# Kernel tuning notes

Measured on AMD Instinct MI355X. Metric: run time of the kernel, lower is better.

Reference implementation:

```python
import jax, jax.numpy as jnp
import numpy as np
from jax import lax

VOCAB = 60      # len(ALL_CHARS): BOS + 52 letters + " .,;'-" + EOS
EMB = 100       # emb_dim
HID = 100       # HIDDEN_SIZE
SEQ = 262144    # long-document sequence length


def setup_inputs() -> dict:
    key = jax.random.key(0)
    k = jax.random.split(key, 6)
    s = 1.0 / np.sqrt(HID)  # PyTorch GRU init scale
    x = jax.random.randint(k[0], (1, SEQ), 0, VOCAB)
    emb = jax.random.normal(k[1], (VOCAB, EMB), dtype=jnp.float32)
    w_ih = jax.random.uniform(k[2], (3 * HID, EMB), minval=-s, maxval=s, dtype=jnp.float32)
    w_hh = jax.random.uniform(k[3], (3 * HID, HID), minval=-s, maxval=s, dtype=jnp.float32)
    b_ih = jax.random.uniform(k[4], (3 * HID,), minval=-s, maxval=s, dtype=jnp.float32)
    b_hh = jax.random.uniform(k[5], (3 * HID,), minval=-s, maxval=s, dtype=jnp.float32)
    return {"x": x, "emb": emb, "w_ih": w_ih, "w_hh": w_hh, "b_ih": b_ih, "b_hh": b_hh}


def reference(x, emb, w_ih, w_hh, b_ih, b_hh):
    # Embedding lookup: [1, S] -> [S, E]  (batch asserted == 1 in original)
    xe = emb[x[0]]
    # Precompute input-side gate projections for all timesteps: [S, 3H]
    xp = xe @ w_ih.T + b_ih
    H = w_hh.shape[1]
    w_hr, w_hz, w_hn = w_hh[:H], w_hh[H:2 * H], w_hh[2 * H:]
    b_hr, b_hz, b_hn = b_hh[:H], b_hh[H:2 * H], b_hh[2 * H:]

    def step(h, xp_t):
        xr, xz, xn = xp_t[:H], xp_t[H:2 * H], xp_t[2 * H:]
        r = jax.nn.sigmoid(xr + h @ w_hr.T + b_hr)
        z = jax.nn.sigmoid(xz + h @ w_hz.T + b_hz)
        n = jnp.tanh(xn + r * (h @ w_hn.T + b_hn))
        h_new = (1.0 - z) * n + z * h
        return h_new, None

    h0 = jnp.zeros((H,), dtype=xp.dtype)
    h_last, _ = lax.scan(step, h0, xp)
    # Match torch GRU h_n shape: [num_layers=1, batch=1, HID]
    return h_last[None, None, :]
```

## Files before the change

### kernel.cpp

```cpp
#include <hip/hip_runtime.h>
#include <stdint.h>

#define VOCAB 60
#define EMB   100
#define HID   100
#define SEQN  262144
#define NPROJ 300
#define HSTR  104
#define NMFW  4
#define MT    6
#define KS    3

typedef float    f32x4 __attribute__((ext_vector_type(4)));
typedef _Float16 h16x2 __attribute__((ext_vector_type(2)));
typedef _Float16 h16x4 __attribute__((ext_vector_type(4)));
typedef _Float16 h16x8 __attribute__((ext_vector_type(8)));

__device__ __forceinline__ float fast_sig(float x) {
    return __builtin_amdgcn_rcpf(1.0f + __builtin_amdgcn_exp2f(-1.442695041f * x));
}
__device__ __forceinline__ float fast_tanh(float x) {
    return 2.0f * __builtin_amdgcn_rcpf(1.0f + __builtin_amdgcn_exp2f(-2.885390082f * x)) - 1.0f;
}

#if __has_builtin(__builtin_amdgcn_fdot2)
#define DOT2(A, B, C) __builtin_amdgcn_fdot2((A), (B), (C), false)
#else
__device__ __forceinline__ float DOT2(h16x2 a, h16x2 b, float c) {
    return fmaf((float)a.x, (float)b.x, fmaf((float)a.y, (float)b.y, c));
}
#endif

#define AS2(U)    __builtin_bit_cast(h16x2, (U))
#define SH2(V, I) __builtin_shufflevector((V), (V), (I), (I) + 1)

__global__ void precompute_kernel(const float* __restrict__ emb,
                                  const float* __restrict__ w_ih,
                                  const float* __restrict__ b_ih,
                                  const float* __restrict__ b_hh,
                                  const float* __restrict__ w_hh,
                                  float* __restrict__ proj,
                                  _Float16* __restrict__ afrag,
                                  _Float16* __restrict__ wtail)
{
    int idx = blockIdx.x * blockDim.x + threadIdx.x;
    if (idx < VOCAB * NPROJ) {
        int v = idx / NPROJ, j = idx - v * NPROJ;
        float acc = b_ih[j] + (j < 2 * HID ? b_hh[j] : 0.0f);
        const float* er = emb  + v * EMB;
        const float* wr = w_ih + j * EMB;
        #pragma unroll 4
        for (int k = 0; k < EMB; ++k) acc = fmaf(er[k], wr[k], acc);
        proj[idx] = acc;
    }
    if (idx < NMFW * MT * KS * 64 * 8) {
        int e    = idx & 7;
        int lane = (idx >> 3) & 63;
        int q0   = idx >> 9;
        int ks   = q0 % KS;
        int q1   = q0 / KS;
        int m    = q1 % MT;
        int w    = q1 / MT;
        int rho  = lane & 15;
        int G    = rho >> 2, q = rho & 3;
        int wh   = m % 3;
        int j    = 32 * w + 8 * G + 2 * q + (m >= 3 ? 1 : 0);
        int k    = ks * 32 + ((lane >> 4) << 3) + e;
        afrag[idx] = (j < HID)
                   ? (_Float16)w_hh[(wh * HID + j) * HID + k] : (_Float16)0.0f;
    }
    if (idx < 3 * HID * 4) {
        int e = idx & 3;
        int row = idx >> 2;
        wtail[idx] = (_Float16)w_hh[row * HID + 96 + e];
    }
}

#define MFMA(A, B, C) __builtin_amdgcn_mfma_f32_16x16x32_f16((A), (B), (C), 0, 0, 0)

#define LOADF(M, K) \
    h16x8 af_##M##_##K = *(const h16x8*)(afrag + ((((wave*MT+(M))*KS+(K))*64) + lane) * 8);

#define PIN(D) asm("v_mov_b32 %0, %0" : "+v"(D));

#define BAR() asm volatile("s_waitcnt lgkmcnt(0)\n\ts_barrier" ::: "memory")

#define B_LOAD(BUF) {                                   \
    const _Float16* hp_ = hbuf[BUF];                    \
    b0  = *(const h16x8*)(hp_ +  0 + ko);               \
    b1  = *(const h16x8*)(hp_ + 32 + ko);               \
    b2  = *(const h16x8*)(hp_ + 64 + ko);               \
    hb4 = *(const h16x4*)(hp_ + 96); }

#define STEP(CUR, NXT, TOKSRC) {                                            \
          \
    asm("" : "+a"(af_0_0), "+a"(af_0_1), "+a"(af_0_2), "+a"(af_1_0), "+a"(af_1_1)); \
    asm("" : "+a"(af_1_2), "+a"(af_2_0), "+a"(af_2_1), "+a"(af_2_2), "+a"(af_3_0)); \
    asm("" : "+a"(af_3_1), "+a"(af_3_2), "+a"(af_4_0), "+a"(af_4_1), "+a"(af_4_2)); \
    asm("" : "+a"(af_5_0), "+a"(af_5_1), "+a"(af_5_2));                     \
           \
    int ts_ = __builtin_amdgcn_readfirstlane(TOKSRC);                       \
    const float* pb_ = projj + ts_ * NPROJ;                                 \
    float xr_n = pb_[0];                                                    \
    float xz_n = pb_[HID];                                                  \
    float xn_n = pb_[2 * HID];                                              \
    h16x2 hb01 = SH2(hb4, 0), hb23 = SH2(hb4, 2);                           \
                                                  \
    f32x4 ac0, ac3;                                                         \
    ac0 = MFMA(af_0_0, b0, zz);  ac3 = MFMA(af_3_0, b0, zz);                \
    ac0 = MFMA(af_0_1, b1, ac0); ac3 = MFMA(af_3_1, b1, ac3);               \
    ac0 = MFMA(af_0_2, b2, ac0); ac3 = MFMA(af_3_2, b2, ac3);               \
                        \
    f32x4 acR = hi ? ac3 : ac0;                                             \
    float sRl = (q2 & 1) ? acR[1] : acR[0], sRh = (q2 & 1) ? acR[3] : acR[2]; \
    float sR  = (q2 & 2) ? sRh : sRl;                                       \
    float tR  = DOT2(AS2(wtR01), hb01, DOT2(AS2(wtR23), hb23, 0.0f));       \
    float r   = fast_sig(sR + tR + xr);                                     \
                                                  \
    f32x4 ac1, ac4;                                                         \
    ac1 = MFMA(af_1_0, b0, zz);  ac4 = MFMA(af_4_0, b0, zz);                \
    ac1 = MFMA(af_1_1, b1, ac1); ac4 = MFMA(af_4_1, b1, ac4);               \
    ac1 = MFMA(af_1_2, b2, ac1); ac4 = MFMA(af_4_2, b2, ac4);               \
    f32x4 acZ = hi ? ac4 : ac1;                                             \
    float sZl = (q2 & 1) ? acZ[1] : acZ[0], sZh = (q2 & 1) ? acZ[3] : acZ[2]; \
    float sZ  = (q2 & 2) ? sZh : sZl;                                       \
    float tZ  = DOT2(AS2(wtZ01), hb01, DOT2(AS2(wtZ23), hb23, 0.0f));       \
    float z   = fast_sig(sZ + tZ + xz);                                     \
                                                  \
    f32x4 ac2, ac5;                                                         \
    ac2 = MFMA(af_2_0, b0, zz);  ac5 = MFMA(af_5_0, b0, zz);                \
    ac2 = MFMA(af_2_1, b1, ac2); ac5 = MFMA(af_5_1, b1, ac5);               \
    ac2 = MFMA(af_2_2, b2, ac2); ac5 = MFMA(af_5_2, b2, ac5);               \
    f32x4 acN = hi ? ac5 : ac2;                                             \
    float sNl = (q2 & 1) ? acN[1] : acN[0], sNh = (q2 & 1) ? acN[3] : acN[2]; \
    float sN  = (q2 & 2) ? sNh : sNl;                                       \
    float tN  = DOT2(AS2(wtN01), hb01, DOT2(AS2(wtN23), hb23, 0.0f));       \
    float n   = fast_tanh(xn + r * (sN + tN + bhn));                        \
    float hnew = n + z * (hold - n);                                        \
    hold = hnew;                                                            \
    if (active) hbuf[NXT][j] = (_Float16)hnew;                              \
    BAR();                                                                  \
    B_LOAD(NXT);                    \
    xr = xr_n;  xz = xz_n;  xn = xn_n; }

__global__ __launch_bounds__(256, 1) __attribute__((amdgpu_waves_per_eu(1, 1)))
void gru_seq_kernel(const int*      __restrict__ x,
                    const float*    __restrict__ b_hh,
                    const float*    __restrict__ proj,
                    const _Float16* __restrict__ afrag,
                    const _Float16* __restrict__ wtail,
                    float*          __restrict__ out)
{
    __shared__ __align__(16) _Float16 hbuf[2][HSTR];

    const int tid  = threadIdx.x;
    const int wave = tid >> 6;
    const int lane = tid & 63;
    const int G    = lane >> 4;
    const int c    = lane & 15;
    const int ko   = (lane >> 4) << 3;

    const int  jv     = 32 * wave + 8 * G + c;
    const bool active = (c < 8) && (jv < HID);
    const int  j      = active ? jv : 0;
    const int  q2     = (c >> 1) & 3;
    const bool hi     = (c & 1);

    if (tid < 2 * HSTR) ((_Float16*)hbuf)[tid] = (_Float16)0.0f;

    LOADF(0,0) LOADF(0,1) LOADF(0,2)
    LOADF(1,0) LOADF(1,1) LOADF(1,2)
    LOADF(2,0) LOADF(2,1) LOADF(2,2)
    LOADF(3,0) LOADF(3,1) LOADF(3,2)
    LOADF(4,0) LOADF(4,1) LOADF(4,2)
    LOADF(5,0) LOADF(5,1) LOADF(5,2)

    const uint32_t* wt32 = (const uint32_t*)wtail;
    uint32_t wtR01 = wt32[(0 * HID + j) * 2],     wtR23 = wt32[(0 * HID + j) * 2 + 1];
    uint32_t wtZ01 = wt32[(1 * HID + j) * 2],     wtZ23 = wt32[(1 * HID + j) * 2 + 1];
    uint32_t wtN01 = wt32[(2 * HID + j) * 2],     wtN23 = wt32[(2 * HID + j) * 2 + 1];
    PIN(wtR01) PIN(wtR23) PIN(wtZ01) PIN(wtZ23) PIN(wtN01) PIN(wtN23)

    const float  bhn   = b_hh[2 * HID + j];
    const float* projj = proj + j;
    float hold = 0.0f;

    int4 qA = *(const int4*)(x);
    int4 qB = *(const int4*)(x + 4);

    int tok0 = __builtin_amdgcn_readfirstlane(qA.x);
    float xr = projj[tok0 * NPROJ];
    float xz = projj[tok0 * NPROJ + HID];
    float xn = projj[tok0 * NPROJ + 2 * HID];

    const f32x4 zz = {0.f, 0.f, 0.f, 0.f};
    h16x8 b0, b1, b2;
    h16x4 hb4;
    __syncthreads();
    B_LOAD(0);

    for (int t = 0; t < SEQN; t += 4) {
        int  ldix = (t + 8 <= SEQN - 4) ? (t + 8) : (SEQN - 4);
        int4 qC   = *(const int4*)(x + ldix);

        STEP(0, 1, qA.y)
        STEP(1, 0, qA.z)
        STEP(0, 1, qA.w)
        STEP(1, 0, qB.x)

        qA = qB;  qB = qC;
    }

    if (active) out[j] = hold;
}

extern "C" void kernel_launch(void* const* d_in, const int* in_sizes, int n_in,
                              void* d_out, int out_size, void* d_ws, size_t ws_size,
                              hipStream_t stream)
{
    const int*   x    = (const int*)  d_in[0];
    const float* emb  = (const float*)d_in[1];
    const float* w_ih = (const float*)d_in[2];
    const float* w_hh = (const float*)d_in[3];
    const float* b_ih = (const float*)d_in[4];
    const float* b_hh = (const float*)d_in[5];
    float* out = (float*)d_out;

    float*    proj  = (float*)d_ws;
    _Float16* afrag = (_Float16*)(proj + VOCAB * NPROJ);
    _Float16* wtail = afrag + NMFW * MT * KS * 64 * 8;

    const int total = NMFW * MT * KS * 64 * 8;
    precompute_kernel<<<(total + 255) / 256, 256, 0, stream>>>(
        emb, w_ih, b_ih, b_hh, w_hh, proj, afrag, wtail);
    gru_seq_kernel<<<1, 256, 0, stream>>>(x, b_hh, proj, afrag, wtail, out);
}
```

Baseline: 93.94 ms.

## Split recurrent GEMV across eight waves with one MFMA chain per gate

The sequential GRU kernel moves from 4 waves that each own 32 hidden units (two MFMA chains per gate) to 8 waves that each own 16 hidden units (one MFMA chain per gate). The weight fragment layout is rebuilt to match, and each lane's output is picked from the accumulator by diagonal selection. The aim is to shorten the per-step MFMA critical path and the register pressure per wave. In exchange, the per-step barrier now has to synchronize twice as many waves, with two waves sharing each SIMD.

Result: slower. 104.1 ms (+10.8%).

```diff
diff --git a/kernel.cpp b/kernel.cpp
--- a/kernel.cpp
+++ b/kernel.cpp
@@ -7,8 +7,8 @@
 #define SEQN  262144
 #define NPROJ 300
 #define HSTR  104
-#define NMFW  4
-#define MT    6
+#define NW    8
+#define MT    3
 #define KS    3
 
 typedef float    f32x4 __attribute__((ext_vector_type(4)));
@@ -53,7 +53,7 @@
         for (int k = 0; k < EMB; ++k) acc = fmaf(er[k], wr[k], acc);
         proj[idx] = acc;
     }
-    if (idx < NMFW * MT * KS * 64 * 8) {
+    if (idx < NW * MT * KS * 64 * 8) {
         int e    = idx & 7;
         int lane = (idx >> 3) & 63;
         int q0   = idx >> 9;
@@ -61,13 +61,10 @@
         int q1   = q0 / KS;
         int m    = q1 % MT;
         int w    = q1 / MT;
-        int rho  = lane & 15;
-        int G    = rho >> 2, q = rho & 3;
-        int wh   = m % 3;
-        int j    = 32 * w + 8 * G + 2 * q + (m >= 3 ? 1 : 0);
+        int j    = 16 * w + (lane & 15);
         int k    = ks * 32 + ((lane >> 4) << 3) + e;
         afrag[idx] = (j < HID)
-                   ? (_Float16)w_hh[(wh * HID + j) * HID + k] : (_Float16)0.0f;
+                   ? (_Float16)w_hh[(m * HID + j) * HID + k] : (_Float16)0.0f;
     }
     if (idx < 3 * HID * 4) {
         int e = idx & 3;
@@ -92,12 +89,15 @@
     b2  = *(const h16x8*)(hp_ + 64 + ko);               \
     hb4 = *(const h16x4*)(hp_ + 96); }
 
+#define MUX(AC, S) {                                    \
+    float lo_ = (qs & 1) ? AC[1] : AC[0];               \
+    float hi_ = (qs & 1) ? AC[3] : AC[2];               \
+    S = (qs & 2) ? hi_ : lo_; }
+
 #define STEP(CUR, NXT, TOKSRC) {                                            \
           \
     asm("" : "+a"(af_0_0), "+a"(af_0_1), "+a"(af_0_2), "+a"(af_1_0), "+a"(af_1_1)); \
-    asm("" : "+a"(af_1_2), "+a"(af_2_0), "+a"(af_2_1), "+a"(af_2_2), "+a"(af_3_0)); \
-    asm("" : "+a"(af_3_1), "+a"(af_3_2), "+a"(af_4_0), "+a"(af_4_1), "+a"(af_4_2)); \
-    asm("" : "+a"(af_5_0), "+a"(af_5_1), "+a"(af_5_2));                     \
+    asm("" : "+a"(af_1_2), "+a"(af_2_0), "+a"(af_2_1), "+a"(af_2_2));       \
            \
     int ts_ = __builtin_amdgcn_readfirstlane(TOKSRC);                       \
     const float* pb_ = projj + ts_ * NPROJ;                                 \
@@ -105,35 +105,28 @@
     float xz_n = pb_[HID];                                                  \
     float xn_n = pb_[2 * HID];                                              \
     h16x2 hb01 = SH2(hb4, 0), hb23 = SH2(hb4, 2);                           \
-                                                  \
-    f32x4 ac0, ac3;                                                         \
-    ac0 = MFMA(af_0_0, b0, zz);  ac3 = MFMA(af_3_0, b0, zz);                \
-    ac0 = MFMA(af_0_1, b1, ac0); ac3 = MFMA(af_3_1, b1, ac3);               \
-    ac0 = MFMA(af_0_2, b2, ac0); ac3 = MFMA(af_3_2, b2, ac3);               \
-                        \
-    f32x4 acR = hi ? ac3 : ac0;                                             \
-    float sRl = (q2 & 1) ? acR[1] : acR[0], sRh = (q2 & 1) ? acR[3] : acR[2]; \
-    float sR  = (q2 & 2) ? sRh : sRl;                                       \
+                    \
+    f32x4 ac0;                                                              \
+    ac0 = MFMA(af_0_0, b0, zz);                                             \
+    ac0 = MFMA(af_0_1, b1, ac0);                                            \
+    ac0 = MFMA(af_0_2, b2, ac0);                                            \
+    float sR; MUX(ac0, sR)                                                  \
     float tR  = DOT2(AS2(wtR01), hb01, DOT2(AS2(wtR23), hb23, 0.0f));       \
     float r   = fast_sig(sR + tR + xr);                                     \
-                                                  \
-    f32x4 ac1, ac4;                                                         \
-    ac1 = MFMA(af_1_0, b0, zz);  ac4 = MFMA(af_4_0, b0, zz);                \
-    ac1 = MFMA(af_1_1, b1, ac1); ac4 = MFMA(af_4_1, b1, ac4);               \
-    ac1 = MFMA(af_1_2, b2, ac1); ac4 = MFMA(af_4_2, b2, ac4);               \
-    f32x4 acZ = hi ? ac4 : ac1;                                             \
-    float sZl = (q2 & 1) ? acZ[1] : acZ[0], sZh = (q2 & 1) ? acZ[3] : acZ[2]; \
-    float sZ  = (q2 & 2) ? sZh : sZl;                                       \
+                                             \
+    f32x4 ac1;                                                              \
+    ac1 = MFMA(af_1_0, b0, zz);                                             \
+    ac1 = MFMA(af_1_1, b1, ac1);                                            \
+    ac1 = MFMA(af_1_2, b2, ac1);                                            \
+    float sZ; MUX(ac1, sZ)                                                  \
     float tZ  = DOT2(AS2(wtZ01), hb01, DOT2(AS2(wtZ23), hb23, 0.0f));       \
     float z   = fast_sig(sZ + tZ + xz);                                     \
-                                                  \
-    f32x4 ac2, ac5;                                                         \
-    ac2 = MFMA(af_2_0, b0, zz);  ac5 = MFMA(af_5_0, b0, zz);                \
-    ac2 = MFMA(af_2_1, b1, ac2); ac5 = MFMA(af_5_1, b1, ac5);               \
-    ac2 = MFMA(af_2_2, b2, ac2); ac5 = MFMA(af_5_2, b2, ac5);               \
-    f32x4 acN = hi ? ac5 : ac2;                                             \
-    float sNl = (q2 & 1) ? acN[1] : acN[0], sNh = (q2 & 1) ? acN[3] : acN[2]; \
-    float sN  = (q2 & 2) ? sNh : sNl;                                       \
+                                        \
+    f32x4 ac2;                                                              \
+    ac2 = MFMA(af_2_0, b0, zz);                                             \
+    ac2 = MFMA(af_2_1, b1, ac2);                                            \
+    ac2 = MFMA(af_2_2, b2, ac2);                                            \
+    float sN; MUX(ac2, sN)                                                  \
     float tN  = DOT2(AS2(wtN01), hb01, DOT2(AS2(wtN23), hb23, 0.0f));       \
     float n   = fast_tanh(xn + r * (sN + tN + bhn));                        \
     float hnew = n + z * (hold - n);                                        \
@@ -143,7 +136,7 @@
     B_LOAD(NXT);                    \
     xr = xr_n;  xz = xz_n;  xn = xn_n; }
 
-__global__ __launch_bounds__(256, 1) __attribute__((amdgpu_waves_per_eu(1, 1)))
+__global__ __launch_bounds__(512, 2) __attribute__((amdgpu_waves_per_eu(2, 2)))
 void gru_seq_kernel(const int*      __restrict__ x,
                     const float*    __restrict__ b_hh,
                     const float*    __restrict__ proj,
@@ -158,22 +151,18 @@
     const int lane = tid & 63;
     const int G    = lane >> 4;
     const int c    = lane & 15;
-    const int ko   = (lane >> 4) << 3;
-
-    const int  jv     = 32 * wave + 8 * G + c;
-    const bool active = (c < 8) && (jv < HID);
+    const int ko   = G << 3;
+    const int qs   = c & 3;
+
+    const int  jv     = 16 * wave + c;
+    const bool active = (G == (c >> 2)) && (jv < HID);
     const int  j      = active ? jv : 0;
-    const int  q2     = (c >> 1) & 3;
-    const bool hi     = (c & 1);
 
     if (tid < 2 * HSTR) ((_Float16*)hbuf)[tid] = (_Float16)0.0f;
 
     LOADF(0,0) LOADF(0,1) LOADF(0,2)
     LOADF(1,0) LOADF(1,1) LOADF(1,2)
     LOADF(2,0) LOADF(2,1) LOADF(2,2)
-    LOADF(3,0) LOADF(3,1) LOADF(3,2)
-    LOADF(4,0) LOADF(4,1) LOADF(4,2)
-    LOADF(5,0) LOADF(5,1) LOADF(5,2)
 
     const uint32_t* wt32 = (const uint32_t*)wtail;
     uint32_t wtR01 = wt32[(0 * HID + j) * 2],     wtR23 = wt32[(0 * HID + j) * 2 + 1];
@@ -228,10 +217,10 @@
 
     float*    proj  = (float*)d_ws;
     _Float16* afrag = (_Float16*)(proj + VOCAB * NPROJ);
-    _Float16* wtail = afrag + NMFW * MT * KS * 64 * 8;
-
-    const int total = NMFW * MT * KS * 64 * 8;
+    _Float16* wtail = afrag + NW * MT * KS * 64 * 8;
+
+    const int total = NW * MT * KS * 64 * 8;
     precompute_kernel<<<(total + 255) / 256, 256, 0, stream>>>(
         emb, w_ih, b_ih, b_hh, w_hh, proj, afrag, wtail);
-    gru_seq_kernel<<<1, 256, 0, stream>>>(x, b_hh, proj, afrag, wtail, out);
-}
+    gru_seq_kernel<<<1, 512, 0, stream>>>(x, b_hh, proj, afrag, wtail, out);
+}
```
